# Kernel tuning notes

Measured on AMD Instinct MI355X. Metric: run time of the kernel, lower is better.

## Reference

```python
import jax, jax.numpy as jnp
import numpy as np

N_NODES = 10000
N_EDGES = 320000
IN_DIM = 128
HID = 256


def setup_inputs() -> dict:
    key = jax.random.key(0)
    ks = jax.random.split(key, 10)
    s_in = 1.0 / np.sqrt(IN_DIM)
    s_h = 1.0 / np.sqrt(HID)
    return {
        "x": jax.random.normal(ks[0], (N_NODES, IN_DIM), dtype=jnp.float32),
        "edge_index": jax.random.randint(ks[1], (2, N_EDGES), 0, N_NODES, dtype=jnp.int64),
        # feature_projector Linear(IN_DIM -> HID)
        "Wp": jax.random.uniform(ks[2], (IN_DIM, HID), jnp.float32, -s_in, s_in),
        "bp": jax.random.uniform(ks[3], (HID,), jnp.float32, -s_in, s_in),
        # LSTM(input=HID, hidden=HID) params, torch layout [4H, H], gate order i,f,g,o
        "W_ih": jax.random.uniform(ks[4], (4 * HID, HID), jnp.float32, -s_h, s_h),
        "W_hh": jax.random.uniform(ks[5], (4 * HID, HID), jnp.float32, -s_h, s_h),
        "b_ih": jax.random.uniform(ks[6], (4 * HID,), jnp.float32, -s_h, s_h),
        "b_hh": jax.random.uniform(ks[7], (4 * HID,), jnp.float32, -s_h, s_h),
        # EvolveGCN-O initial weight [H, H] (glorot-style)
        "initial_weight": jax.random.normal(ks[8], (HID, HID), dtype=jnp.float32) * np.sqrt(2.0 / (2 * HID)),
        # GCNConv bias
        "b_gcn": jnp.zeros((HID,), dtype=jnp.float32),
    }


def _forward(x, edge_index, Wp, bp, W_ih, W_hh, b_ih, b_hh, initial_weight, b_gcn):
    n = x.shape[0]
    # 1) feature projection
    h = x @ Wp + bp  # [N, H]
    # 2) EvolveGCN-O: one LSTM step on the weight matrix (rows = batch),
    #    with h0 = c0 = initial_weight; evolved hidden state is the GCN weight.
    gates = initial_weight @ W_ih.T + b_ih + initial_weight @ W_hh.T + b_hh  # [H, 4H]
    i_g, f_g, g_g, o_g = jnp.split(gates, 4, axis=-1)
    c = jax.nn.sigmoid(f_g) * initial_weight + jax.nn.sigmoid(i_g) * jnp.tanh(g_g)
    W = jax.nn.sigmoid(o_g) * jnp.tanh(c)  # [H, H]
    # 3) GCN propagation with fixed W: out = D^{-1/2}(A+I)D^{-1/2} (h W) + b
    hw = h @ W  # [N, H]
    self_loop = jnp.arange(n, dtype=edge_index.dtype)
    src = jnp.concatenate([edge_index[0], self_loop])
    dst = jnp.concatenate([edge_index[1], self_loop])
    ones = jnp.ones(src.shape[0], dtype=hw.dtype)
    deg = jax.ops.segment_sum(ones, dst, num_segments=n)  # in-degree incl. self loop
    dinv = jnp.where(deg > 0, jax.lax.rsqrt(deg), 0.0)
    norm = dinv[src] * dinv[dst]  # [E+N]
    out = jax.ops.segment_sum(hw[src] * norm[:, None], dst, num_segments=n)
    return out + b_gcn


def reference(x, edge_index, Wp, bp, W_ih, W_hh, b_ih, b_hh, initial_weight, b_gcn):
    return _forward(x, edge_index, Wp, bp, W_ih, W_hh, b_ih, b_hh, initial_weight, b_gcn)
```

## Files before the change

### kernel.cpp

```cpp
#include <hip/hip_runtime.h>
#include <math.h>

#define N_NODES 10000
#define N_EDGES 320000
#define IN_DIM  128
#define HID     256
#define CAP     128
#define NB1     512
#define NWB     64
#define NFB     (NB1 - NWB)

typedef __attribute__((ext_vector_type(8))) short frag_ab;
typedef __attribute__((ext_vector_type(4))) float frag_cd;


__device__ __forceinline__ unsigned bf16rne(float f) {
    union { float f; unsigned u; } c; c.f = f;
    return (c.u + 0x7FFFu + ((c.u >> 16) & 1u)) >> 16;
}
__device__ __forceinline__ float sig_f(float x)  { return 1.f / (1.f + __expf(-x)); }
__device__ __forceinline__ float tanh_f(float x) { return 1.f - 2.f / (1.f + __expf(2.f * x)); }

__global__ __launch_bounds__(256, 2)
void k1_prep(const int* __restrict__ ei,
             const float* __restrict__ Wp, const float* __restrict__ bp,
             const float* __restrict__ wih, const float* __restrict__ whh,
             const float* __restrict__ b_ih, const float* __restrict__ b_hh,
             const float* __restrict__ iw,
             int* __restrict__ cursor, unsigned* __restrict__ wct,
             float* __restrict__ bc, int* __restrict__ bucket) {
    __shared__ __align__(16) char smem_raw[54784];
    const int bid = blockIdx.x;
    const int t = threadIdx.x;

    if (bid < NWB) {
        float (*aT)[260]  = (float(*)[260])smem_raw;
        float (*bSt)[20]  = (float(*)[20])(smem_raw + 33280);
        #pragma unroll
        for (int n = 0; n < 16; ++n) {
            int nrow = (n >> 2) * 256 + 4 * bid + (n & 3);
            bSt[t][n] = wih[nrow * 256 + t] + whh[nrow * 256 + t];
        }
        int mg = t >> 2, ng = t & 3;
        float acc[4][4] = {};
        for (int kt = 0; kt < 8; ++kt) {
            int k0 = kt * 32;
            __syncthreads();
            #pragma unroll
            for (int c = 0; c < 8; ++c) {
                float4 v = *(const float4*)&iw[t * 256 + k0 + 4 * c];
                aT[4 * c + 0][t] = v.x; aT[4 * c + 1][t] = v.y;
                aT[4 * c + 2][t] = v.z; aT[4 * c + 3][t] = v.w;
            }
            __syncthreads();
            #pragma unroll 4
            for (int kk = 0; kk < 32; ++kk) {
                float4 a4 = *(const float4*)&aT[kk][4 * mg];
                float4 b4 = *(const float4*)&bSt[k0 + kk][4 * ng];
                float a[4] = {a4.x, a4.y, a4.z, a4.w};
                float b[4] = {b4.x, b4.y, b4.z, b4.w};
                #pragma unroll
                for (int i = 0; i < 4; ++i)
                    #pragma unroll
                    for (int j = 0; j < 4; ++j)
                        acc[i][j] = fmaf(a[i], b[j], acc[i][j]);
            }
        }
        float (*gates_lds)[17] = (float(*)[17])smem_raw;
        float (*wevc)[260]     = (float(*)[260])(smem_raw + 33280);
        __syncthreads();
        #pragma unroll
        for (int i = 0; i < 4; ++i)
            #pragma unroll
            for (int j = 0; j < 4; ++j)
                gates_lds[4 * mg + i][4 * ng + j] = acc[i][j];
        __syncthreads();
        {
            int r = t;
            #pragma unroll
            for (int jj = 0; jj < 4; ++jj) {
                int jcol = 4 * bid + jj;
                float gi = gates_lds[r][0  + jj] + b_ih[jcol]       + b_hh[jcol];
                float gf = gates_lds[r][4  + jj] + b_ih[256 + jcol] + b_hh[256 + jcol];
                float gg = gates_lds[r][8  + jj] + b_ih[512 + jcol] + b_hh[512 + jcol];
                float go = gates_lds[r][12 + jj] + b_ih[768 + jcol] + b_hh[768 + jcol];
                float c  = sig_f(gf) * iw[r * 256 + jcol] + sig_f(gi) * tanh_f(gg);
                wevc[jj][r] = sig_f(go) * tanh_f(c);
            }
        }
        __syncthreads();
        {
            int a2 = t & 63, jj = t >> 6;
            float c0 = 0.f, c1 = 0.f;
            const float* p0 = &Wp[(2 * a2) * 256];
            const float* p1 = &Wp[(2 * a2 + 1) * 256];
            #pragma unroll 4
            for (int k4 = 0; k4 < 64; ++k4) {
                float4 w4 = *(const float4*)&wevc[jj][4 * k4];
                float4 q0 = *(const float4*)&p0[4 * k4];
                float4 q1 = *(const float4*)&p1[4 * k4];
                c0 = fmaf(q0.x, w4.x, fmaf(q0.y, w4.y, fmaf(q0.z, w4.z, fmaf(q0.w, w4.w, c0))));
                c1 = fmaf(q1.x, w4.x, fmaf(q1.y, w4.y, fmaf(q1.z, w4.z, fmaf(q1.w, w4.w, c1))));
            }
            wct[(4 * bid + jj) * 64 + a2] = bf16rne(c0) | (bf16rne(c1) << 16);
            if (t < 4) {
                float s = 0.f;
                for (int k4 = 0; k4 < 64; ++k4) {
                    float4 b4 = *(const float4*)&bp[4 * k4];
                    float4 w4 = *(const float4*)&wevc[t][4 * k4];
                    s = fmaf(b4.x, w4.x, fmaf(b4.y, w4.y, fmaf(b4.z, w4.z, fmaf(b4.w, w4.w, s))));
                }
                bc[4 * bid + t] = s;
            }
        }
    } else {
        for (int u = (bid - NWB) * 256 + t; u < N_EDGES / 4; u += NFB * 256) {
            int4 s4 = *(const int4*)&ei[u * 4];
            int4 d4 = *(const int4*)&ei[N_EDGES + u * 4];
            int p0 = atomicAdd(&cursor[d4.x], 1);
            if (p0 < CAP) bucket[d4.x * CAP + p0] = s4.x;
            int p1 = atomicAdd(&cursor[d4.y], 1);
            if (p1 < CAP) bucket[d4.y * CAP + p1] = s4.y;
            int p2 = atomicAdd(&cursor[d4.z], 1);
            if (p2 < CAP) bucket[d4.z * CAP + p2] = s4.z;
            int p3 = atomicAdd(&cursor[d4.w], 1);
            if (p3 < CAP) bucket[d4.w * CAP + p3] = s4.w;
        }
    }
}

__global__ __launch_bounds__(256)
void k2_agg_out(const float* __restrict__ x, const int* __restrict__ cursor,
                const int* __restrict__ bucket, const unsigned* __restrict__ wct,
                const float* __restrict__ bc, const float* __restrict__ b_gcn,
                float* __restrict__ out) {
    __shared__ unsigned y_lds[16][64];
    __shared__ float rs_lds[16];
    const int t = threadIdx.x;
    const int tile = blockIdx.x;
    const int w = t >> 6, lane = t & 63;
    const int q = lane >> 4, ln = lane & 15;
    const float2* x2 = (const float2*)x;

    for (int vi = 0; vi < 4; ++vi) {
        int r = vi * 4 + w;
        int v = tile * 16 + r;
        int cntv = cursor[v];
        float dv = rsqrtf((float)(cntv + 1));
        int cnt2 = cntv > CAP ? CAP : cntv;
        float2 sv = x2[v * 64 + lane];
        float acc0 = dv * sv.x, acc1 = dv * sv.y, wsum = dv;
        const int4* bkt4 = (const int4*)&bucket[v * CAP];
        int j = 0;
        for (; j + 8 <= cnt2; j += 8) {
            int4 sa = bkt4[j >> 2];
            int4 sb = bkt4[(j >> 2) + 1];
            float w0 = rsqrtf((float)(cursor[sa.x] + 1));
            float w1 = rsqrtf((float)(cursor[sa.y] + 1));
            float w2 = rsqrtf((float)(cursor[sa.z] + 1));
            float w3 = rsqrtf((float)(cursor[sa.w] + 1));
            float w4 = rsqrtf((float)(cursor[sb.x] + 1));
            float w5 = rsqrtf((float)(cursor[sb.y] + 1));
            float w6 = rsqrtf((float)(cursor[sb.z] + 1));
            float w7 = rsqrtf((float)(cursor[sb.w] + 1));
            float2 r0 = x2[sa.x * 64 + lane];
            float2 r1 = x2[sa.y * 64 + lane];
            float2 r2 = x2[sa.z * 64 + lane];
            float2 r3 = x2[sa.w * 64 + lane];
            float2 r4 = x2[sb.x * 64 + lane];
            float2 r5 = x2[sb.y * 64 + lane];
            float2 r6 = x2[sb.z * 64 + lane];
            float2 r7 = x2[sb.w * 64 + lane];
            acc0 = fmaf(w0, r0.x, acc0); acc1 = fmaf(w0, r0.y, acc1);
            acc0 = fmaf(w1, r1.x, acc0); acc1 = fmaf(w1, r1.y, acc1);
            acc0 = fmaf(w2, r2.x, acc0); acc1 = fmaf(w2, r2.y, acc1);
            acc0 = fmaf(w3, r3.x, acc0); acc1 = fmaf(w3, r3.y, acc1);
            acc0 = fmaf(w4, r4.x, acc0); acc1 = fmaf(w4, r4.y, acc1);
            acc0 = fmaf(w5, r5.x, acc0); acc1 = fmaf(w5, r5.y, acc1);
            acc0 = fmaf(w6, r6.x, acc0); acc1 = fmaf(w6, r6.y, acc1);
            acc0 = fmaf(w7, r7.x, acc0); acc1 = fmaf(w7, r7.y, acc1);
            wsum += w0 + w1 + w2 + w3 + w4 + w5 + w6 + w7;
        }
        for (; j < cnt2; ++j) {
            int s = bucket[v * CAP + j];
            float ws = rsqrtf((float)(cursor[s] + 1));
            float2 rv = x2[s * 64 + lane];
            acc0 = fmaf(ws, rv.x, acc0); acc1 = fmaf(ws, rv.y, acc1);
            wsum += ws;
        }
        y_lds[r][lane] = bf16rne(dv * acc0) | (bf16rne(dv * acc1) << 16);
        if (lane == 0) rs_lds[r] = dv * wsum;
    }
    __syncthreads();

    const int4* ya   = (const int4*)&y_lds[0][0];
    const int4* wct4 = (const int4*)wct;
    union { int4 v; frag_ab f; } a[4];
    #pragma unroll
    for (int kc = 0; kc < 4; ++kc)
        a[kc].v = ya[ln * 16 + kc * 4 + q];
    float rsv[4];
    #pragma unroll
    for (int r = 0; r < 4; ++r) rsv[r] = rs_lds[q * 4 + r];
    #pragma unroll
    for (int i = 0; i < 4; ++i) {
        int n0 = (w + 4 * i) * 16;
        union { int4 v; frag_ab f; } b[4];
        #pragma unroll
        for (int kc = 0; kc < 4; ++kc)
            b[kc].v = wct4[(n0 + ln) * 16 + kc * 4 + q];
        frag_cd accd = {0.f, 0.f, 0.f, 0.f};
        #pragma unroll
        for (int kc = 0; kc < 4; ++kc)
            accd = __builtin_amdgcn_mfma_f32_16x16x32_bf16(a[kc].f, b[kc].f, accd, 0, 0, 0);
        int n = n0 + ln;
        float bcv = bc[n], bgv = b_gcn[n];
        #pragma unroll
        for (int r = 0; r < 4; ++r) {
            int m = tile * 16 + q * 4 + r;
            out[m * HID + n] = accd[r] + rsv[r] * bcv + bgv;
        }
    }
}

extern "C" void kernel_launch(void* const* d_in, const int* in_sizes, int n_in,
                              void* d_out, int out_size, void* d_ws, size_t ws_size,
                              hipStream_t stream) {
    const float* x     = (const float*)d_in[0];
    const int*   ei    = (const int*)d_in[1];
    const float* Wp    = (const float*)d_in[2];
    const float* bp    = (const float*)d_in[3];
    const float* W_ih  = (const float*)d_in[4];
    const float* W_hh  = (const float*)d_in[5];
    const float* b_ih  = (const float*)d_in[6];
    const float* b_hh  = (const float*)d_in[7];
    const float* iw    = (const float*)d_in[8];
    const float* b_gcn = (const float*)d_in[9];
    float* out = (float*)d_out;

    char* ws = (char*)d_ws;
    int*      cursor = (int*)     (ws + 0);
    unsigned* wct    = (unsigned*)(ws + 40064);
    float*    bc     = (float*)   (ws + 105600);
    int*      bucket = (int*)     (ws + 106624);

    hipMemsetAsync(cursor, 0, N_NODES * sizeof(int), stream);

    k1_prep<<<NB1, 256, 0, stream>>>(ei, Wp, bp, W_ih, W_hh, b_ih, b_hh, iw,
                                     cursor, wct, bc, bucket);
    k2_agg_out<<<625, 256, 0, stream>>>(x, cursor, bucket, wct, bc, b_gcn, out);
}
```

Before: 161.7 us.

## Replace global atomic edge bucketing with LDS histograms and a cross-block prefix

Edge bucketing drops global per-edge atomics and runs on 10 blocks instead. Each block first builds a shared-memory histogram of destination counts for its edge slice and publishes it. The blocks then meet at a spin-wait flag, compute per-block base offsets and total counts, and scatter sources using only LDS atomics. Separately, the LSTM weight path now loads initial_weight with coalesced reads, caches its gate columns in LDS, and tiles Wp through LDS. Only 10 blocks now do the edge work, and the spin barrier assumes all 10 are co-resident.

New measurement: 166.7 us. 3.1% more time.

```diff
diff --git a/kernel.cpp b/kernel.cpp
--- a/kernel.cpp
+++ b/kernel.cpp
@@ -6,9 +6,11 @@
 #define IN_DIM  128
 #define HID     256
 #define CAP     128
-#define NB1     512
 #define NWB     64
-#define NFB     (NB1 - NWB)
+#define NFB     10
+#define NB1     (NWB + NFB)
+#define EPB     (N_EDGES / NFB)
+#define QPB     (EPB / 4)
 
 typedef __attribute__((ext_vector_type(8))) short frag_ab;
 typedef __attribute__((ext_vector_type(4))) float frag_cd;
@@ -20,6 +22,23 @@
 }
 __device__ __forceinline__ float sig_f(float x)  { return 1.f / (1.f + __expf(-x)); }
 __device__ __forceinline__ float tanh_f(float x) { return 1.f - 2.f / (1.f + __expf(2.f * x)); }
+
+__device__ __forceinline__ void wt_u32(unsigned* p, unsigned v) {
+    __hip_atomic_store(p, v, __ATOMIC_RELAXED, __HIP_MEMORY_SCOPE_AGENT);
+}
+__device__ __forceinline__ void arrive(int* c) {
+    __syncthreads();
+    if (threadIdx.x == 0)
+        __hip_atomic_fetch_add(c, 1, __ATOMIC_RELAXED, __HIP_MEMORY_SCOPE_AGENT);
+}
+__device__ __forceinline__ void waitflag(int* c, int n) {
+    if (threadIdx.x == 0) {
+        while (__hip_atomic_load(c, __ATOMIC_RELAXED, __HIP_MEMORY_SCOPE_AGENT) < n)
+            __builtin_amdgcn_s_sleep(2);
+    }
+    __syncthreads();
+    asm volatile("" ::: "memory");
+}
 
 __global__ __launch_bounds__(256, 2)
 void k1_prep(const int* __restrict__ ei,
@@ -27,32 +46,41 @@
              const float* __restrict__ wih, const float* __restrict__ whh,
              const float* __restrict__ b_ih, const float* __restrict__ b_hh,
              const float* __restrict__ iw,
-             int* __restrict__ cursor, unsigned* __restrict__ wct,
-             float* __restrict__ bc, int* __restrict__ bucket) {
-    __shared__ __align__(16) char smem_raw[54784];
+             int* __restrict__ cursor, int* __restrict__ flag,
+             unsigned* __restrict__ wct, float* __restrict__ bc,
+             unsigned* __restrict__ histG, int* __restrict__ bucket) {
+    __shared__ __align__(16) char smem_raw[57920];
     const int bid = blockIdx.x;
     const int t = threadIdx.x;
 
     if (bid < NWB) {
         float (*aT)[260]  = (float(*)[260])smem_raw;
         float (*bSt)[20]  = (float(*)[20])(smem_raw + 33280);
+        float (*iwc)[260] = (float(*)[260])(smem_raw + 53760);
         #pragma unroll
         for (int n = 0; n < 16; ++n) {
             int nrow = (n >> 2) * 256 + 4 * bid + (n & 3);
             bSt[t][n] = wih[nrow * 256 + t] + whh[nrow * 256 + t];
         }
-        int mg = t >> 2, ng = t & 3;
+        const int mg = t >> 2, ng = t & 3;
+        const int srow = t >> 3, sf4 = t & 7;
         float acc[4][4] = {};
         for (int kt = 0; kt < 8; ++kt) {
             int k0 = kt * 32;
             __syncthreads();
             #pragma unroll
-            for (int c = 0; c < 8; ++c) {
-                float4 v = *(const float4*)&iw[t * 256 + k0 + 4 * c];
-                aT[4 * c + 0][t] = v.x; aT[4 * c + 1][t] = v.y;
-                aT[4 * c + 2][t] = v.z; aT[4 * c + 3][t] = v.w;
+            for (int rr = 0; rr < 8; ++rr) {
+                int row = srow + 32 * rr;
+                float4 v = *(const float4*)&iw[row * 256 + k0 + 4 * sf4];
+                aT[4 * sf4 + 0][row] = v.x; aT[4 * sf4 + 1][row] = v.y;
+                aT[4 * sf4 + 2][row] = v.z; aT[4 * sf4 + 3][row] = v.w;
             }
             __syncthreads();
+            if (kt == (bid >> 3)) {
+                int c0 = (4 * bid) & 31;
+                #pragma unroll
+                for (int jj = 0; jj < 4; ++jj) iwc[jj][t] = aT[c0 + jj][t];
+            }
             #pragma unroll 4
             for (int kk = 0; kk < 32; ++kk) {
                 float4 a4 = *(const float4*)&aT[kk][4 * mg];
@@ -84,47 +112,91 @@
                 float gf = gates_lds[r][4  + jj] + b_ih[256 + jcol] + b_hh[256 + jcol];
                 float gg = gates_lds[r][8  + jj] + b_ih[512 + jcol] + b_hh[512 + jcol];
                 float go = gates_lds[r][12 + jj] + b_ih[768 + jcol] + b_hh[768 + jcol];
-                float c  = sig_f(gf) * iw[r * 256 + jcol] + sig_f(gi) * tanh_f(gg);
+                float c  = sig_f(gf) * iwc[jj][r] + sig_f(gi) * tanh_f(gg);
                 wevc[jj][r] = sig_f(go) * tanh_f(c);
             }
         }
-        __syncthreads();
-        {
-            int a2 = t & 63, jj = t >> 6;
-            float c0 = 0.f, c1 = 0.f;
-            const float* p0 = &Wp[(2 * a2) * 256];
-            const float* p1 = &Wp[(2 * a2 + 1) * 256];
+        float (*wpT)[132] = (float(*)[132])smem_raw;
+        const int a2 = t & 63, jj = t >> 6;
+        float c0 = 0.f, c1 = 0.f;
+        for (int kt2 = 0; kt2 < 8; ++kt2) {
+            int k0 = kt2 * 32;
+            __syncthreads();
+            #pragma unroll
+            for (int ri = 0; ri < 4; ++ri) {
+                int a = srow + 32 * ri;
+                float4 v = *(const float4*)&Wp[a * 256 + k0 + 4 * sf4];
+                wpT[4 * sf4 + 0][a] = v.x; wpT[4 * sf4 + 1][a] = v.y;
+                wpT[4 * sf4 + 2][a] = v.z; wpT[4 * sf4 + 3][a] = v.w;
+            }
+            __syncthreads();
+            #pragma unroll 8
+            for (int kk = 0; kk < 32; ++kk) {
+                float2 wv = *(const float2*)&wpT[kk][2 * a2];
+                float wev = wevc[jj][k0 + kk];
+                c0 = fmaf(wv.x, wev, c0);
+                c1 = fmaf(wv.y, wev, c1);
+            }
+        }
+        wct[(4 * bid + jj) * 64 + a2] = bf16rne(c0) | (bf16rne(c1) << 16);
+        if (t < 4) {
+            float s = 0.f;
             #pragma unroll 4
             for (int k4 = 0; k4 < 64; ++k4) {
-                float4 w4 = *(const float4*)&wevc[jj][4 * k4];
-                float4 q0 = *(const float4*)&p0[4 * k4];
-                float4 q1 = *(const float4*)&p1[4 * k4];
-                c0 = fmaf(q0.x, w4.x, fmaf(q0.y, w4.y, fmaf(q0.z, w4.z, fmaf(q0.w, w4.w, c0))));
-                c1 = fmaf(q1.x, w4.x, fmaf(q1.y, w4.y, fmaf(q1.z, w4.z, fmaf(q1.w, w4.w, c1))));
-            }
-            wct[(4 * bid + jj) * 64 + a2] = bf16rne(c0) | (bf16rne(c1) << 16);
-            if (t < 4) {
-                float s = 0.f;
-                for (int k4 = 0; k4 < 64; ++k4) {
-                    float4 b4 = *(const float4*)&bp[4 * k4];
-                    float4 w4 = *(const float4*)&wevc[t][4 * k4];
-                    s = fmaf(b4.x, w4.x, fmaf(b4.y, w4.y, fmaf(b4.z, w4.z, fmaf(b4.w, w4.w, s))));
-                }
-                bc[4 * bid + t] = s;
-            }
+                float4 b4 = *(const float4*)&bp[4 * k4];
+                float4 w4 = *(const float4*)&wevc[t][4 * k4];
+                s = fmaf(b4.x, w4.x, fmaf(b4.y, w4.y, fmaf(b4.z, w4.z, fmaf(b4.w, w4.w, s))));
+            }
+            bc[4 * bid + t] = s;
         }
     } else {
-        for (int u = (bid - NWB) * 256 + t; u < N_EDGES / 4; u += NFB * 256) {
-            int4 s4 = *(const int4*)&ei[u * 4];
-            int4 d4 = *(const int4*)&ei[N_EDGES + u * 4];
-            int p0 = atomicAdd(&cursor[d4.x], 1);
-            if (p0 < CAP) bucket[d4.x * CAP + p0] = s4.x;
-            int p1 = atomicAdd(&cursor[d4.y], 1);
-            if (p1 < CAP) bucket[d4.y * CAP + p1] = s4.y;
-            int p2 = atomicAdd(&cursor[d4.z], 1);
-            if (p2 < CAP) bucket[d4.z * CAP + p2] = s4.z;
-            int p3 = atomicAdd(&cursor[d4.w], 1);
-            if (p3 < CAP) bucket[d4.w * CAP + p3] = s4.w;
+        const int fb = bid - NWB;
+        unsigned* hist = (unsigned*)smem_raw;
+        for (int i = t; i < N_NODES; i += 256) hist[i] = 0;
+        __syncthreads();
+        const int* dsts = ei + N_EDGES;
+        const int q0 = fb * QPB;
+        #pragma unroll 4
+        for (int it = 0; it < 32; ++it) {
+            int idx = it * 256 + t;
+            if (idx < QPB) {
+                int4 d4 = *(const int4*)&dsts[(q0 + idx) * 4];
+                atomicAdd(&hist[d4.x], 1u);
+                atomicAdd(&hist[d4.y], 1u);
+                atomicAdd(&hist[d4.z], 1u);
+                atomicAdd(&hist[d4.w], 1u);
+            }
+        }
+        __syncthreads();
+        for (int i = t; i < N_NODES; i += 256)
+            wt_u32(&histG[fb * N_NODES + i], hist[i]);
+        arrive(flag);
+        waitflag(flag, NFB);
+        #pragma unroll 4
+        for (int i = t; i < N_NODES; i += 256) {
+            unsigned base = 0, total = 0;
+            #pragma unroll
+            for (int b = 0; b < NFB; ++b) {
+                unsigned h = histG[b * N_NODES + i];
+                base += (b < fb) ? h : 0u;
+                total += h;
+            }
+            hist[i] = base;
+            if ((unsigned)(i - fb * 1000) < 1000u) cursor[i] = (int)total;
+        }
+        __syncthreads();
+        #pragma unroll 4
+        for (int it = 0; it < 32; ++it) {
+            int idx = it * 256 + t;
+            if (idx < QPB) {
+                int4 s4 = *(const int4*)&ei[(q0 + idx) * 4];
+                int4 d4 = *(const int4*)&dsts[(q0 + idx) * 4];
+                unsigned p;
+                p = atomicAdd(&hist[d4.x], 1u); if (p < CAP) bucket[d4.x * CAP + p] = s4.x;
+                p = atomicAdd(&hist[d4.y], 1u); if (p < CAP) bucket[d4.y * CAP + p] = s4.y;
+                p = atomicAdd(&hist[d4.z], 1u); if (p < CAP) bucket[d4.z * CAP + p] = s4.z;
+                p = atomicAdd(&hist[d4.w], 1u); if (p < CAP) bucket[d4.w * CAP + p] = s4.w;
+            }
         }
     }
 }
@@ -240,13 +312,15 @@
 
     char* ws = (char*)d_ws;
     int*      cursor = (int*)     (ws + 0);
+    int*      flag   = (int*)     (ws + 40000);
     unsigned* wct    = (unsigned*)(ws + 40064);
     float*    bc     = (float*)   (ws + 105600);
-    int*      bucket = (int*)     (ws + 106624);
-
-    hipMemsetAsync(cursor, 0, N_NODES * sizeof(int), stream);
+    unsigned* histG  = (unsigned*)(ws + 106624);
+    int*      bucket = (int*)     (ws + 506624);
+
+    hipMemsetAsync(flag, 0, 16, stream);
 
     k1_prep<<<NB1, 256, 0, stream>>>(ei, Wp, bp, W_ih, W_hh, b_ih, b_hh, iw,
-                                     cursor, wct, bc, bucket);
+                                     cursor, flag, wct, bc, histG, bucket);
     k2_agg_out<<<625, 256, 0, stream>>>(x, cursor, bucket, wct, bc, b_gcn, out);
 }
```

## Gather bf16-packed features in aggregation and restage prep loads through LDS

Applied to the files above, without the earlier changes.

Adds a third group of blocks to the prep kernel that converts x to packed bf16, so the aggregation kernel gathers half as many bytes per neighbor row and widens each value back to fp32 with shifts. The weight-evolution blocks also get coalesced row-wise loads of the initial weight, cache the needed initial-weight columns in LDS, and stage Wp transposed through LDS instead of reading it strided from global memory. The cost is an extra 2.5 MB workspace write and read of bf16 features, and lower input precision in the gather.

Result: faster. 150.4 us (-7.0%).

```diff
diff --git a/kernel.cpp b/kernel.cpp
--- a/kernel.cpp
+++ b/kernel.cpp
@@ -6,9 +6,10 @@
 #define IN_DIM  128
 #define HID     256
 #define CAP     128
-#define NB1     512
 #define NWB     64
-#define NFB     (NB1 - NWB)
+#define NFB     448
+#define NXB     128
+#define NB1     (NWB + NFB + NXB)
 
 typedef __attribute__((ext_vector_type(8))) short frag_ab;
 typedef __attribute__((ext_vector_type(4))) float frag_cd;
@@ -22,37 +23,46 @@
 __device__ __forceinline__ float tanh_f(float x) { return 1.f - 2.f / (1.f + __expf(2.f * x)); }
 
 __global__ __launch_bounds__(256, 2)
-void k1_prep(const int* __restrict__ ei,
+void k1_prep(const float* __restrict__ x, const int* __restrict__ ei,
              const float* __restrict__ Wp, const float* __restrict__ bp,
              const float* __restrict__ wih, const float* __restrict__ whh,
              const float* __restrict__ b_ih, const float* __restrict__ b_hh,
              const float* __restrict__ iw,
              int* __restrict__ cursor, unsigned* __restrict__ wct,
-             float* __restrict__ bc, int* __restrict__ bucket) {
-    __shared__ __align__(16) char smem_raw[54784];
+             float* __restrict__ bc, unsigned* __restrict__ xb,
+             int* __restrict__ bucket) {
+    __shared__ __align__(16) char smem_raw[57920];
     const int bid = blockIdx.x;
     const int t = threadIdx.x;
 
     if (bid < NWB) {
         float (*aT)[260]  = (float(*)[260])smem_raw;
         float (*bSt)[20]  = (float(*)[20])(smem_raw + 33280);
+        float (*iwc)[260] = (float(*)[260])(smem_raw + 53760);
         #pragma unroll
         for (int n = 0; n < 16; ++n) {
             int nrow = (n >> 2) * 256 + 4 * bid + (n & 3);
             bSt[t][n] = wih[nrow * 256 + t] + whh[nrow * 256 + t];
         }
-        int mg = t >> 2, ng = t & 3;
+        const int mg = t >> 2, ng = t & 3;
+        const int srow = t >> 3, sf4 = t & 7;
         float acc[4][4] = {};
         for (int kt = 0; kt < 8; ++kt) {
             int k0 = kt * 32;
             __syncthreads();
             #pragma unroll
-            for (int c = 0; c < 8; ++c) {
-                float4 v = *(const float4*)&iw[t * 256 + k0 + 4 * c];
-                aT[4 * c + 0][t] = v.x; aT[4 * c + 1][t] = v.y;
-                aT[4 * c + 2][t] = v.z; aT[4 * c + 3][t] = v.w;
-            }
-            __syncthreads();
+            for (int rr = 0; rr < 8; ++rr) {
+                int row = srow + 32 * rr;
+                float4 v = *(const float4*)&iw[row * 256 + k0 + 4 * sf4];
+                aT[4 * sf4 + 0][row] = v.x; aT[4 * sf4 + 1][row] = v.y;
+                aT[4 * sf4 + 2][row] = v.z; aT[4 * sf4 + 3][row] = v.w;
+            }
+            __syncthreads();
+            if (kt == (bid >> 3)) {
+                int c0 = (4 * bid) & 31;
+                #pragma unroll
+                for (int jj = 0; jj < 4; ++jj) iwc[jj][t] = aT[c0 + jj][t];
+            }
             #pragma unroll 4
             for (int kk = 0; kk < 32; ++kk) {
                 float4 a4 = *(const float4*)&aT[kk][4 * mg];
@@ -84,36 +94,44 @@
                 float gf = gates_lds[r][4  + jj] + b_ih[256 + jcol] + b_hh[256 + jcol];
                 float gg = gates_lds[r][8  + jj] + b_ih[512 + jcol] + b_hh[512 + jcol];
                 float go = gates_lds[r][12 + jj] + b_ih[768 + jcol] + b_hh[768 + jcol];
-                float c  = sig_f(gf) * iw[r * 256 + jcol] + sig_f(gi) * tanh_f(gg);
+                float c  = sig_f(gf) * iwc[jj][r] + sig_f(gi) * tanh_f(gg);
                 wevc[jj][r] = sig_f(go) * tanh_f(c);
             }
         }
-        __syncthreads();
-        {
-            int a2 = t & 63, jj = t >> 6;
-            float c0 = 0.f, c1 = 0.f;
-            const float* p0 = &Wp[(2 * a2) * 256];
-            const float* p1 = &Wp[(2 * a2 + 1) * 256];
+        float (*wpT)[132] = (float(*)[132])smem_raw;
+        const int a2 = t & 63, jj = t >> 6;
+        float c0 = 0.f, c1 = 0.f;
+        for (int kt2 = 0; kt2 < 8; ++kt2) {
+            int k0 = kt2 * 32;
+            __syncthreads();
+            #pragma unroll
+            for (int ri = 0; ri < 4; ++ri) {
+                int a = srow + 32 * ri;
+                float4 v = *(const float4*)&Wp[a * 256 + k0 + 4 * sf4];
+                wpT[4 * sf4 + 0][a] = v.x; wpT[4 * sf4 + 1][a] = v.y;
+                wpT[4 * sf4 + 2][a] = v.z; wpT[4 * sf4 + 3][a] = v.w;
+            }
+            __syncthreads();
+            #pragma unroll 8
+            for (int kk = 0; kk < 32; ++kk) {
+                float2 wv = *(const float2*)&wpT[kk][2 * a2];
+                float wev = wevc[jj][k0 + kk];
+                c0 = fmaf(wv.x, wev, c0);
+                c1 = fmaf(wv.y, wev, c1);
+            }
+        }
+        wct[(4 * bid + jj) * 64 + a2] = bf16rne(c0) | (bf16rne(c1) << 16);
+        if (t < 4) {
+            float s = 0.f;
             #pragma unroll 4
             for (int k4 = 0; k4 < 64; ++k4) {
-                float4 w4 = *(const float4*)&wevc[jj][4 * k4];
-                float4 q0 = *(const float4*)&p0[4 * k4];
-                float4 q1 = *(const float4*)&p1[4 * k4];
-                c0 = fmaf(q0.x, w4.x, fmaf(q0.y, w4.y, fmaf(q0.z, w4.z, fmaf(q0.w, w4.w, c0))));
-                c1 = fmaf(q1.x, w4.x, fmaf(q1.y, w4.y, fmaf(q1.z, w4.z, fmaf(q1.w, w4.w, c1))));
-            }
-            wct[(4 * bid + jj) * 64 + a2] = bf16rne(c0) | (bf16rne(c1) << 16);
-            if (t < 4) {
-                float s = 0.f;
-                for (int k4 = 0; k4 < 64; ++k4) {
-                    float4 b4 = *(const float4*)&bp[4 * k4];
-                    float4 w4 = *(const float4*)&wevc[t][4 * k4];
-                    s = fmaf(b4.x, w4.x, fmaf(b4.y, w4.y, fmaf(b4.z, w4.z, fmaf(b4.w, w4.w, s))));
-                }
-                bc[4 * bid + t] = s;
-            }
-        }
-    } else {
+                float4 b4 = *(const float4*)&bp[4 * k4];
+                float4 w4 = *(const float4*)&wevc[t][4 * k4];
+                s = fmaf(b4.x, w4.x, fmaf(b4.y, w4.y, fmaf(b4.z, w4.z, fmaf(b4.w, w4.w, s))));
+            }
+            bc[4 * bid + t] = s;
+        }
+    } else if (bid < NWB + NFB) {
         for (int u = (bid - NWB) * 256 + t; u < N_EDGES / 4; u += NFB * 256) {
             int4 s4 = *(const int4*)&ei[u * 4];
             int4 d4 = *(const int4*)&ei[N_EDGES + u * 4];
@@ -126,11 +144,19 @@
             int p3 = atomicAdd(&cursor[d4.w], 1);
             if (p3 < CAP) bucket[d4.w * CAP + p3] = s4.w;
         }
+    } else {
+        const float4* x4 = (const float4*)x;
+        uint2* xb2 = (uint2*)xb;
+        for (int idx = (bid - NWB - NFB) * 256 + t; idx < N_NODES * 32; idx += NXB * 256) {
+            float4 v = x4[idx];
+            xb2[idx] = make_uint2(bf16rne(v.x) | (bf16rne(v.y) << 16),
+                                  bf16rne(v.z) | (bf16rne(v.w) << 16));
+        }
     }
 }
 
 __global__ __launch_bounds__(256)
-void k2_agg_out(const float* __restrict__ x, const int* __restrict__ cursor,
+void k2_agg_out(const unsigned* __restrict__ xb, const int* __restrict__ cursor,
                 const int* __restrict__ bucket, const unsigned* __restrict__ wct,
                 const float* __restrict__ bc, const float* __restrict__ b_gcn,
                 float* __restrict__ out) {
@@ -140,7 +166,6 @@
     const int tile = blockIdx.x;
     const int w = t >> 6, lane = t & 63;
     const int q = lane >> 4, ln = lane & 15;
-    const float2* x2 = (const float2*)x;
 
     for (int vi = 0; vi < 4; ++vi) {
         int r = vi * 4 + w;
@@ -148,8 +173,10 @@
         int cntv = cursor[v];
         float dv = rsqrtf((float)(cntv + 1));
         int cnt2 = cntv > CAP ? CAP : cntv;
-        float2 sv = x2[v * 64 + lane];
-        float acc0 = dv * sv.x, acc1 = dv * sv.y, wsum = dv;
+        unsigned self = xb[v * 64 + lane];
+        union { unsigned u; float f; } c0, c1;
+        c0.u = self << 16; c1.u = self & 0xFFFF0000u;
+        float acc0 = dv * c0.f, acc1 = dv * c1.f, wsum = dv;
         const int4* bkt4 = (const int4*)&bucket[v * CAP];
         int j = 0;
         for (; j + 8 <= cnt2; j += 8) {
@@ -163,29 +190,40 @@
             float w5 = rsqrtf((float)(cursor[sb.y] + 1));
             float w6 = rsqrtf((float)(cursor[sb.z] + 1));
             float w7 = rsqrtf((float)(cursor[sb.w] + 1));
-            float2 r0 = x2[sa.x * 64 + lane];
-            float2 r1 = x2[sa.y * 64 + lane];
-            float2 r2 = x2[sa.z * 64 + lane];
-            float2 r3 = x2[sa.w * 64 + lane];
-            float2 r4 = x2[sb.x * 64 + lane];
-            float2 r5 = x2[sb.y * 64 + lane];
-            float2 r6 = x2[sb.z * 64 + lane];
-            float2 r7 = x2[sb.w * 64 + lane];
-            acc0 = fmaf(w0, r0.x, acc0); acc1 = fmaf(w0, r0.y, acc1);
-            acc0 = fmaf(w1, r1.x, acc0); acc1 = fmaf(w1, r1.y, acc1);
-            acc0 = fmaf(w2, r2.x, acc0); acc1 = fmaf(w2, r2.y, acc1);
-            acc0 = fmaf(w3, r3.x, acc0); acc1 = fmaf(w3, r3.y, acc1);
-            acc0 = fmaf(w4, r4.x, acc0); acc1 = fmaf(w4, r4.y, acc1);
-            acc0 = fmaf(w5, r5.x, acc0); acc1 = fmaf(w5, r5.y, acc1);
-            acc0 = fmaf(w6, r6.x, acc0); acc1 = fmaf(w6, r6.y, acc1);
-            acc0 = fmaf(w7, r7.x, acc0); acc1 = fmaf(w7, r7.y, acc1);
+            unsigned r0 = xb[sa.x * 64 + lane];
+            unsigned r1 = xb[sa.y * 64 + lane];
+            unsigned r2 = xb[sa.z * 64 + lane];
+            unsigned r3 = xb[sa.w * 64 + lane];
+            unsigned r4 = xb[sb.x * 64 + lane];
+            unsigned r5 = xb[sb.y * 64 + lane];
+            unsigned r6 = xb[sb.z * 64 + lane];
+            unsigned r7 = xb[sb.w * 64 + lane];
+            union { unsigned u; float f; } a0, a1;
+            a0.u = r0 << 16; a1.u = r0 & 0xFFFF0000u;
+            acc0 = fmaf(w0, a0.f, acc0); acc1 = fmaf(w0, a1.f, acc1);
+            a0.u = r1 << 16; a1.u = r1 & 0xFFFF0000u;
+            acc0 = fmaf(w1, a0.f, acc0); acc1 = fmaf(w1, a1.f, acc1);
+            a0.u = r2 << 16; a1.u = r2 & 0xFFFF0000u;
+            acc0 = fmaf(w2, a0.f, acc0); acc1 = fmaf(w2, a1.f, acc1);
+            a0.u = r3 << 16; a1.u = r3 & 0xFFFF0000u;
+            acc0 = fmaf(w3, a0.f, acc0); acc1 = fmaf(w3, a1.f, acc1);
+            a0.u = r4 << 16; a1.u = r4 & 0xFFFF0000u;
+            acc0 = fmaf(w4, a0.f, acc0); acc1 = fmaf(w4, a1.f, acc1);
+            a0.u = r5 << 16; a1.u = r5 & 0xFFFF0000u;
+            acc0 = fmaf(w5, a0.f, acc0); acc1 = fmaf(w5, a1.f, acc1);
+            a0.u = r6 << 16; a1.u = r6 & 0xFFFF0000u;
+            acc0 = fmaf(w6, a0.f, acc0); acc1 = fmaf(w6, a1.f, acc1);
+            a0.u = r7 << 16; a1.u = r7 & 0xFFFF0000u;
+            acc0 = fmaf(w7, a0.f, acc0); acc1 = fmaf(w7, a1.f, acc1);
             wsum += w0 + w1 + w2 + w3 + w4 + w5 + w6 + w7;
         }
         for (; j < cnt2; ++j) {
             int s = bucket[v * CAP + j];
             float ws = rsqrtf((float)(cursor[s] + 1));
-            float2 rv = x2[s * 64 + lane];
-            acc0 = fmaf(ws, rv.x, acc0); acc1 = fmaf(ws, rv.y, acc1);
+            unsigned rr = xb[s * 64 + lane];
+            union { unsigned u; float f; } a0, a1;
+            a0.u = rr << 16; a1.u = rr & 0xFFFF0000u;
+            acc0 = fmaf(ws, a0.f, acc0); acc1 = fmaf(ws, a1.f, acc1);
             wsum += ws;
         }
         y_lds[r][lane] = bf16rne(dv * acc0) | (bf16rne(dv * acc1) << 16);
@@ -242,11 +280,12 @@
     int*      cursor = (int*)     (ws + 0);
     unsigned* wct    = (unsigned*)(ws + 40064);
     float*    bc     = (float*)   (ws + 105600);
-    int*      bucket = (int*)     (ws + 106624);
+    unsigned* xb     = (unsigned*)(ws + 106624);
+    int*      bucket = (int*)     (ws + 2666624);
 
     hipMemsetAsync(cursor, 0, N_NODES * sizeof(int), stream);
 
-    k1_prep<<<NB1, 256, 0, stream>>>(ei, Wp, bp, W_ih, W_hh, b_ih, b_hh, iw,
-                                     cursor, wct, bc, bucket);
-    k2_agg_out<<<625, 256, 0, stream>>>(x, cursor, bucket, wct, bc, b_gcn, out);
-}
+    k1_prep<<<NB1, 256, 0, stream>>>(x, ei, Wp, bp, W_ih, W_hh, b_ih, b_hh, iw,
+                                     cursor, wct, bc, xb, bucket);
+    k2_agg_out<<<625, 256, 0, stream>>>(xb, cursor, bucket, wct, bc, b_gcn, out);
+}
```
